# Optimization experiments

Hardware: AMD Instinct MI355X
Metric: run time of the kernel (lower is better)

## Reference

```python
import jax, jax.numpy as jnp
import numpy as np

B, T, D, E, H = 4, 2048, 1024, 4, 8
EPS = 1e-5


def _uniform(k, shape, bound):
    return jax.random.uniform(k, shape, jnp.float32, -bound, bound)


def setup_inputs() -> dict:
    key = jax.random.key(0)
    ks = jax.random.split(key, 12)
    wb = np.sqrt(6.0 / D) / np.sqrt(6.0)  # kaiming_uniform(a=sqrt5) bound ~ 1/sqrt(D)... keep simple
    wb = 1.0 / np.sqrt(D)
    return {
        "x": jax.random.normal(ks[0], (B, T, D), jnp.float32),
        "router_prob": jax.random.uniform(ks[1], (B, T, E), jnp.float32),
        "norm_w": jnp.ones((D,), jnp.float32),
        "norm_b": jnp.zeros((D,), jnp.float32),
        "q_w": _uniform(ks[2], (D, D), wb),
        "q_b": _uniform(ks[3], (D,), wb),
        "k_w": _uniform(ks[4], (D, D), wb),
        "k_b": _uniform(ks[5], (D,), wb),
        "v_w": _uniform(ks[6], (D, D), wb),
        "v_b": _uniform(ks[7], (D,), wb),
        "o_w": _uniform(ks[8], (D, D), wb),
        "o_b": _uniform(ks[9], (D,), wb),
    }


def _layernorm(x, w, b):
    mu = jnp.mean(x, axis=-1, keepdims=True)
    var = jnp.mean(jnp.square(x - mu), axis=-1, keepdims=True)
    return (x - mu) * jax.lax.rsqrt(var + EPS) * w + b


def reference(x, router_prob, norm_w, norm_b, q_w, q_b, k_w, k_b, v_w, v_b, o_w, o_b):
    e_cnt = router_prob.shape[2]
    b, t, d = x.shape
    n = t // e_cnt
    h = H
    scale = d ** (-0.5)  # note: original uses model_dim**-0.5, not head_dim

    qs, ks_, vs = [], [], []
    for e in range(e_cnt):
        xe = x[:, e * n:(e + 1) * n, :]
        xn = _layernorm(xe, norm_w, norm_b)
        m = d // (2 ** e)
        xm = xn[..., :m]  # [b, n, m] matryoshka slice
        # F.linear(xm, W[:, :m], bias): out = xm @ W[:, :m]^T + b -> [b, n, d]
        qs.append(jnp.einsum('bnm,dm->bnd', xm, q_w[:, :m]) + q_b)
        ks_.append(jnp.einsum('bnm,dm->bnd', xm, k_w[:, :m]) + k_b)
        vs.append(jnp.einsum('bnm,dm->bnd', xm, v_w[:, :m]) + v_b)
    q = jnp.concatenate(qs, axis=1)
    k = jnp.concatenate(ks_, axis=1)
    v = jnp.concatenate(vs, axis=1)

    dh = d // h
    q = q.reshape(b, t, h, dh).transpose(0, 2, 1, 3)  # b h t dh
    k = k.reshape(b, t, h, dh).transpose(0, 2, 1, 3)
    v = v.reshape(b, t, h, dh).transpose(0, 2, 1, 3)

    attn = jnp.einsum('bhqd,bhkd->bhqk', q, k) * scale
    attn = jax.nn.softmax(attn, axis=-1)  # dropout = identity in eval
    attn_out = jnp.einsum('bhqk,bhkd->bhqd', attn, v)
    attn_out = attn_out.transpose(0, 2, 1, 3).reshape(b, t, d)

    outs = []
    for e in range(e_cnt):
        sl = slice(e * n, (e + 1) * n)
        m = d // (2 ** e)
        xm = attn_out[:, sl, :m]
        out = jnp.einsum('bnm,om->bno', xm, o_w[:m, :m]) + o_b[:m]  # [b, n, m]
        pad = d - m
        if pad:
            out = jnp.pad(out, ((0, 0), (0, 0), (0, pad)))
        outs.append(out + x[:, sl, :])
    return jnp.concatenate(outs, axis=1)
```

## Files before the change

kernel.cpp:

```cpp
#include <hip/hip_runtime.h>
#include <hip/hip_bf16.h>

#define DEV static __device__ __forceinline__

typedef __attribute__((ext_vector_type(4))) float f32x4;
typedef __attribute__((ext_vector_type(8))) short s16x8;
typedef __attribute__((ext_vector_type(4))) unsigned int u32x4;

constexpr int Bn = 4, Tn = 2048, Dn = 1024, Hn = 8, DH = 128;
constexpr float EPSF = 1e-5f;
constexpr float QSCALE = 0.0450842200277801f;

DEV unsigned short f2bf(float f) {
    unsigned int u = __float_as_uint(f);
    u += 0x7FFF + ((u >> 16) & 1);
    return (unsigned short)(u >> 16);
}

DEV f32x4 mfma16(s16x8 a, s16x8 b, f32x4 c) {
    return __builtin_amdgcn_mfma_f32_16x16x32_bf16(a, b, c, 0, 0, 0);
}

DEV float ex2(float x) {
    float r;
    asm("v_exp_f32 %0, %1" : "=v"(r) : "v"(x));
    return r;
}

DEV unsigned int cvtpk(float lo, float hi) {
    unsigned int r;
    asm("v_cvt_pk_bf16_f32 %0, %1, %2" : "=v"(r) : "v"(lo), "v"(hi));
    return r;
}

typedef __attribute__((address_space(1))) const unsigned int GU32;
typedef __attribute__((address_space(3))) unsigned int LU32;
DEV void gload16(const void* g, void* l) {
    __builtin_amdgcn_global_load_lds((GU32*)g, (LU32*)l, 16, 0, 0);
}

__global__ __launch_bounds__(256) void cvtln_kernel(const float* __restrict__ x,
                                                    const float* __restrict__ w,
                                                    const float* __restrict__ b,
                                                    const float* __restrict__ qw,
                                                    const float* __restrict__ kw,
                                                    const float* __restrict__ vw,
                                                    const float* __restrict__ ow,
                                                    unsigned short* __restrict__ xn,
                                                    unsigned short* __restrict__ wb) {
    int bid = blockIdx.x;
    int tid = threadIdx.x;
    if (bid >= 8192) {
        int base = (bid - 8192) * 1024 + tid * 4;
        #pragma unroll
        for (int j = 0; j < 4; j++) {
            int idx = base + j;
            int sel = idx >> 20;
            int off = idx & (Dn * Dn - 1);
            const float* src = sel == 0 ? qw : sel == 1 ? kw : sel == 2 ? vw : ow;
            wb[idx] = f2bf(src[off]);
        }
        return;
    }
    int tok = bid;
    const float* xp = x + (size_t)tok * Dn;
    float4 v = ((const float4*)xp)[tid];
    float s = v.x + v.y + v.z + v.w;
    float q = v.x * v.x + v.y * v.y + v.z * v.z + v.w * v.w;
    for (int off = 32; off; off >>= 1) {
        s += __shfl_xor(s, off);
        q += __shfl_xor(q, off);
    }
    __shared__ float red[8];
    __shared__ float stats[2];
    int wid = tid >> 6, lane = tid & 63;
    if (lane == 0) { red[wid] = s; red[4 + wid] = q; }
    __syncthreads();
    if (tid == 0) {
        float ts = red[0] + red[1] + red[2] + red[3];
        float tq = red[4] + red[5] + red[6] + red[7];
        float mu = ts / Dn;
        float var = tq / Dn - mu * mu;
        stats[0] = mu;
        stats[1] = rsqrtf(var + EPSF);
    }
    __syncthreads();
    float mu = stats[0], rs = stats[1];
    int c = tid * 4;
    ushort4 o;
    o.x = f2bf((v.x - mu) * rs * w[c + 0] + b[c + 0]);
    o.y = f2bf((v.y - mu) * rs * w[c + 1] + b[c + 1]);
    o.z = f2bf((v.z - mu) * rs * w[c + 2] + b[c + 2]);
    o.w = f2bf((v.w - mu) * rs * w[c + 3] + b[c + 3]);
    ((ushort4*)(xn + (size_t)tok * Dn))[tid] = o;
}

__global__ __launch_bounds__(256) void qkv_gemm(const unsigned short* __restrict__ xn,
                                                const unsigned short* __restrict__ wmat,
                                                const float* __restrict__ qb_,
                                                const float* __restrict__ kb_,
                                                const float* __restrict__ vb_,
                                                unsigned short* __restrict__ outq,
                                                unsigned short* __restrict__ outk,
                                                unsigned short* __restrict__ vt) {
    int rowbase = blockIdx.x * 128;
    int colbase = blockIdx.y * 128;
    int matid = blockIdx.z;
    const unsigned short* W = wmat + (size_t)matid * Dn * Dn;
    const float* bias = matid == 0 ? qb_ : matid == 1 ? kb_ : vb_;
    float oscale = matid == 0 ? QSCALE : 1.0f;
    int e = (rowbase & (Tn - 1)) >> 9;
    int m = Dn >> e;
    int nt = m >> 5;

    __shared__ alignas(16) unsigned short At[3][128 * 32];
    __shared__ alignas(16) unsigned short Bt[3][128 * 32];

    int tid = threadIdx.x;
    int lane = tid & 63, wv = tid >> 6;
    int wr = (wv >> 1) * 64, wc = (wv & 1) * 64;
    int fr = lane & 15, fg = lane >> 4;
    int srow = tid >> 2, scol = (tid & 3) * 8;
    const unsigned short* ga0 = xn + (size_t)(rowbase + srow) * Dn + scol;
    const unsigned short* ga1 = xn + (size_t)(rowbase + 64 + srow) * Dn + scol;
    const unsigned short* gb0 = W + (size_t)(colbase + srow) * Dn + scol;
    const unsigned short* gb1 = W + (size_t)(colbase + 64 + srow) * Dn + scol;

    f32x4 acc[4][4] = {};

    auto STAGE = [&](int tt, int buf) {
        int kk = tt * 32;
        gload16(ga0 + kk, &At[buf][tid * 8]);
        gload16(ga1 + kk, &At[buf][2048 + tid * 8]);
        gload16(gb0 + kk, &Bt[buf][tid * 8]);
        gload16(gb1 + kk, &Bt[buf][2048 + tid * 8]);
    };

    STAGE(0, 0);
    if (nt > 1) STAGE(1, 1);

    int cur = 0, nxt2 = 2;
    for (int t = 0; t < nt; t++) {
        if (t + 1 < nt) { asm volatile("s_waitcnt vmcnt(4)" ::: "memory"); }
        else            { asm volatile("s_waitcnt vmcnt(0)" ::: "memory"); }
        __builtin_amdgcn_s_barrier();
        if (t + 2 < nt) STAGE(t + 2, nxt2);
        s16x8 a[4], b[4];
        #pragma unroll
        for (int i = 0; i < 4; i++) a[i] = *(const s16x8*)&At[cur][(wr + i * 16 + fr) * 32 + fg * 8];
        #pragma unroll
        for (int j = 0; j < 4; j++) b[j] = *(const s16x8*)&Bt[cur][(wc + j * 16 + fr) * 32 + fg * 8];
        #pragma unroll
        for (int i = 0; i < 4; i++)
            #pragma unroll
            for (int j = 0; j < 4; j++) acc[i][j] = mfma16(a[i], b[j], acc[i][j]);
        cur = cur == 2 ? 0 : cur + 1;
        nxt2 = nxt2 == 2 ? 0 : nxt2 + 1;
    }

    if (matid == 2) {
        #pragma unroll
        for (int i = 0; i < 4; i++)
            #pragma unroll
            for (int j = 0; j < 4; j++) {
                int col = colbase + wc + j * 16 + fr;
                float bv = bias[col];
                int row0 = rowbase + wr + i * 16 + fg * 4;
                int bb = row0 >> 11, tl = row0 & (Tn - 1);
                int w32 = tl & 31;
                int tlp = (tl & ~31) | (((w32 >> 2) & 3) * 8 + ((w32 >> 4) & 1) * 4);
                size_t base = (((size_t)bb * Hn + (col >> 7)) * DH + (col & (DH - 1))) * Tn + tlp;
                ushort4 o;
                o.x = f2bf(acc[i][j][0] + bv);
                o.y = f2bf(acc[i][j][1] + bv);
                o.z = f2bf(acc[i][j][2] + bv);
                o.w = f2bf(acc[i][j][3] + bv);
                *(ushort4*)&vt[base] = o;
            }
    } else {
        unsigned short* out = matid == 0 ? outq : outk;
        #pragma unroll
        for (int i = 0; i < 4; i++)
            #pragma unroll
            for (int j = 0; j < 4; j++) {
                int col = colbase + wc + j * 16 + fr;
                float bv = bias[col];
                #pragma unroll
                for (int r = 0; r < 4; r++) {
                    int row = rowbase + wr + i * 16 + fg * 4 + r;
                    out[(size_t)row * Dn + col] = f2bf((acc[i][j][r] + bv) * oscale);
                }
            }
    }
}

__global__ __launch_bounds__(256, 2) void attn_kernel(const unsigned short* __restrict__ Q,
                                                      const unsigned short* __restrict__ K,
                                                      const unsigned short* __restrict__ VT,
                                                      unsigned short* __restrict__ AO) {
    int f = blockIdx.x;
    int qi = f >> 5;
    int bh = f & 31;
    int b = bh >> 3, h = bh & 7;
    int qbase = qi * 128;
    int tid = threadIdx.x;
    int wv = tid >> 6, lane = tid & 63;
    int fr = lane & 15, fg = lane >> 4;

    __shared__ alignas(16) unsigned short Kt[3][32 * 128];
    __shared__ alignas(16) unsigned short Vt[3][64 * 64];

    s16x8 bq[2][4];
    #pragma unroll
    for (int hh = 0; hh < 2; hh++) {
        const size_t qr = ((size_t)b * Tn + qbase + wv * 32 + hh * 16 + fr) * Dn + h * DH;
        #pragma unroll
        for (int c = 0; c < 4; c++) bq[hh][c] = *(const s16x8*)&Q[qr + c * 32 + fg * 8];
    }

    const s16x8 ones = {(short)0x3F80, (short)0x3F80, (short)0x3F80, (short)0x3F80,
                        (short)0x3F80, (short)0x3F80, (short)0x3F80, (short)0x3F80};

    f32x4 acc[2][9] = {};
    float m_run[2] = {-1e30f, -1e30f};

    const unsigned short* Kbase = K + (size_t)b * Tn * Dn + h * DH;
    const unsigned short* Vbase = VT + ((size_t)b * Hn + h) * DH * Tn;

    int k_row_lo = tid >> 4, k_chk = tid & 15;
    int v_row_lo = tid >> 3, v_s = tid & 7;

    auto STAGE = [&](int t) {
        int kb = t * 32;
        int buf = t % 3;
        #pragma unroll
        for (int p = 0; p < 2; p++) {
            int row = p * 16 + k_row_lo;
            int chunk = k_chk ^ (row & 7);
            gload16(Kbase + (size_t)(kb + row) * Dn + chunk * 8,
                    &Kt[buf][p * 2048 + tid * 8]);
        }
        #pragma unroll
        for (int p = 0; p < 2; p++) {
            int row = p * 32 + v_row_lo;
            int c = v_s ^ (row & 7);
            int hi = c >> 2, fgc = c & 3;
            gload16(Vbase + (size_t)(hi * 64 + row) * Tn + kb + fgc * 8,
                    &Vt[buf][p * 2048 + tid * 8]);
        }
    };

    STAGE(0);
    STAGE(1);

    constexpr int NT = Tn / 32;
    int cur = 0;
    for (int t = 0; t < NT; t++) {
        if (t + 1 < NT) { asm volatile("s_waitcnt vmcnt(4)" ::: "memory"); }
        else            { asm volatile("s_waitcnt vmcnt(0)" ::: "memory"); }
        __builtin_amdgcn_s_barrier();
        if (t + 2 < NT) STAGE(t + 2);

        const unsigned short* KtC = &Kt[cur][0];
        const unsigned short* VtC = &Vt[cur][0];

        f32x4 s[2][2] = {};
        __builtin_amdgcn_s_setprio(1);
        #pragma unroll
        for (int c = 0; c < 4; c++) {
            #pragma unroll
            for (int kt = 0; kt < 2; kt++) {
                s16x8 ak = *(const s16x8*)&KtC[(kt * 16 + fr) * 128 +
                                               (((c * 4 + fg) ^ (fr & 7)) * 8)];
                s[0][kt] = mfma16(ak, bq[0][c], s[0][kt]);
                s[1][kt] = mfma16(ak, bq[1][c], s[1][kt]);
            }
        }
        __builtin_amdgcn_s_setprio(0);

        float mx[2];
        #pragma unroll
        for (int hh = 0; hh < 2; hh++) {
            float v = fmaxf(fmaxf(fmaxf(s[hh][0][0], s[hh][0][1]),
                                  fmaxf(s[hh][0][2], s[hh][0][3])),
                            fmaxf(fmaxf(s[hh][1][0], s[hh][1][1]),
                                  fmaxf(s[hh][1][2], s[hh][1][3])));
            v = fmaxf(v, __shfl_xor(v, 16));
            v = fmaxf(v, __shfl_xor(v, 32));
            mx[hh] = v;
        }

        if (!__all(mx[0] - m_run[0] <= 8.0f && mx[1] - m_run[1] <= 8.0f)) {
            #pragma unroll
            for (int hh = 0; hh < 2; hh++) {
                float mnew = fmaxf(m_run[hh], mx[hh]);
                float fsc = ex2(m_run[hh] - mnew);
                float fw[4];
                #pragma unroll
                for (int r = 0; r < 4; r++) fw[r] = __shfl(fsc, fg * 4 + r);
                #pragma unroll
                for (int n = 0; n < 9; n++)
                    #pragma unroll
                    for (int r = 0; r < 4; r++) acc[hh][n][r] *= fw[r];
                m_run[hh] = mnew;
            }
        }

        s16x8 pa[2];
        #pragma unroll
        for (int hh = 0; hh < 2; hh++) {
            float p[8];
            #pragma unroll
            for (int kt = 0; kt < 2; kt++)
                #pragma unroll
                for (int r = 0; r < 4; r++) p[kt * 4 + r] = ex2(s[hh][kt][r] - m_run[hh]);
            u32x4 pw;
            pw.x = cvtpk(p[0], p[1]);
            pw.y = cvtpk(p[2], p[3]);
            pw.z = cvtpk(p[4], p[5]);
            pw.w = cvtpk(p[6], p[7]);
            pa[hh] = __builtin_bit_cast(s16x8, pw);
        }

        __builtin_amdgcn_s_setprio(1);
        #pragma unroll
        for (int n = 0; n < 8; n++) {
            int row = (n & 3) * 16 + fr;
            int hi = n >> 2;
            s16x8 bv = *(const s16x8*)&VtC[row * 64 +
                                           (((hi * 4 + fg) ^ (row & 7)) * 8)];
            acc[0][n] = mfma16(pa[0], bv, acc[0][n]);
            acc[1][n] = mfma16(pa[1], bv, acc[1][n]);
        }
        acc[0][8] = mfma16(pa[0], ones, acc[0][8]);
        acc[1][8] = mfma16(pa[1], ones, acc[1][8]);
        __builtin_amdgcn_s_setprio(0);

        cur = cur == 2 ? 0 : cur + 1;
    }

    #pragma unroll
    for (int hh = 0; hh < 2; hh++) {
        float rl[4];
        #pragma unroll
        for (int r = 0; r < 4; r++) rl[r] = 1.0f / acc[hh][8][r];
        size_t orow0 = ((size_t)b * Tn + qbase + wv * 32 + hh * 16) * Dn + h * DH;
        for (int n = 0; n < 8; n++)
            for (int r = 0; r < 4; r++) {
                float v = acc[hh][n][r] * rl[r];
                AO[orow0 + (size_t)(fg * 4 + r) * Dn + n * 16 + fr] = f2bf(v);
            }
    }
}

__global__ __launch_bounds__(256) void oproj_gemm(const unsigned short* __restrict__ A,
                                                  const unsigned short* __restrict__ W,
                                                  const float* __restrict__ bias,
                                                  const float* __restrict__ x,
                                                  float* __restrict__ out) {
    int rowbase = blockIdx.x * 128;
    int colbase = blockIdx.y * 128;
    int e = (rowbase & (Tn - 1)) >> 9;
    int m = Dn >> e;
    int tid = threadIdx.x;

    if (colbase >= m) {
        #pragma unroll
        for (int i = 0; i < 16; i++) {
            int idx = i * 256 + tid;
            int r = idx >> 5, c4 = (idx & 31) * 4;
            size_t g = (size_t)(rowbase + r) * Dn + colbase + c4;
            *(float4*)&out[g] = *(const float4*)&x[g];
        }
        return;
    }

    __shared__ alignas(16) unsigned short At[3][128 * 32];
    __shared__ alignas(16) unsigned short Bt[3][128 * 32];
    int lane = tid & 63, wv = tid >> 6;
    int wr = (wv >> 1) * 64, wc = (wv & 1) * 64;
    int fr = lane & 15, fg = lane >> 4;
    int srow = tid >> 2, scol = (tid & 3) * 8;
    const unsigned short* ga0 = A + (size_t)(rowbase + srow) * Dn + scol;
    const unsigned short* ga1 = A + (size_t)(rowbase + 64 + srow) * Dn + scol;
    const unsigned short* gb0 = W + (size_t)(colbase + srow) * Dn + scol;
    const unsigned short* gb1 = W + (size_t)(colbase + 64 + srow) * Dn + scol;
    int nt = m >> 5;

    f32x4 acc[4][4] = {};

    auto STAGE = [&](int tt, int buf) {
        int kk = tt * 32;
        gload16(ga0 + kk, &At[buf][tid * 8]);
        gload16(ga1 + kk, &At[buf][2048 + tid * 8]);
        gload16(gb0 + kk, &Bt[buf][tid * 8]);
        gload16(gb1 + kk, &Bt[buf][2048 + tid * 8]);
    };

    STAGE(0, 0);
    if (nt > 1) STAGE(1, 1);

    int cur = 0, nxt2 = 2;
    for (int t = 0; t < nt; t++) {
        if (t + 1 < nt) { asm volatile("s_waitcnt vmcnt(4)" ::: "memory"); }
        else            { asm volatile("s_waitcnt vmcnt(0)" ::: "memory"); }
        __builtin_amdgcn_s_barrier();
        if (t + 2 < nt) STAGE(t + 2, nxt2);
        s16x8 a[4], b[4];
        #pragma unroll
        for (int i = 0; i < 4; i++) a[i] = *(const s16x8*)&At[cur][(wr + i * 16 + fr) * 32 + fg * 8];
        #pragma unroll
        for (int j = 0; j < 4; j++) b[j] = *(const s16x8*)&Bt[cur][(wc + j * 16 + fr) * 32 + fg * 8];
        #pragma unroll
        for (int i = 0; i < 4; i++)
            #pragma unroll
            for (int j = 0; j < 4; j++) acc[i][j] = mfma16(a[i], b[j], acc[i][j]);
        cur = cur == 2 ? 0 : cur + 1;
        nxt2 = nxt2 == 2 ? 0 : nxt2 + 1;
    }

    #pragma unroll
    for (int i = 0; i < 4; i++)
        #pragma unroll
        for (int j = 0; j < 4; j++) {
            int col = colbase + wc + j * 16 + fr;
            float bv = bias[col];
            #pragma unroll
            for (int r = 0; r < 4; r++) {
                int row = rowbase + wr + i * 16 + fg * 4 + r;
                size_t g = (size_t)row * Dn + col;
                out[g] = acc[i][j][r] + bv + x[g];
            }
        }
}

extern "C" void kernel_launch(void* const* d_in, const int* in_sizes, int n_in,
                              void* d_out, int out_size, void* d_ws, size_t ws_size,
                              hipStream_t stream) {
    const float* x   = (const float*)d_in[0];
    const float* nw  = (const float*)d_in[2];
    const float* nb  = (const float*)d_in[3];
    const float* qw  = (const float*)d_in[4];
    const float* qb_ = (const float*)d_in[5];
    const float* kw  = (const float*)d_in[6];
    const float* kb_ = (const float*)d_in[7];
    const float* vw  = (const float*)d_in[8];
    const float* vb_ = (const float*)d_in[9];
    const float* ow  = (const float*)d_in[10];
    const float* ob_ = (const float*)d_in[11];
    float* out = (float*)d_out;

    unsigned short* ws = (unsigned short*)d_ws;
    const size_t NTOK = (size_t)Bn * Tn;
    unsigned short* xn = ws;
    unsigned short* qd = xn + NTOK * Dn;
    unsigned short* kd = qd + NTOK * Dn;
    unsigned short* vt = kd + NTOK * Dn;
    unsigned short* ao = vt + NTOK * Dn;
    unsigned short* wb = ao + NTOK * Dn;

    hipLaunchKernelGGL(cvtln_kernel, dim3(12288), dim3(256), 0, stream,
                       x, nw, nb, qw, kw, vw, ow, xn, wb);
    hipLaunchKernelGGL(qkv_gemm, dim3(64, 8, 3), dim3(256), 0, stream,
                       xn, wb, qb_, kb_, vb_, qd, kd, vt);
    hipLaunchKernelGGL(attn_kernel, dim3(512), dim3(256), 0, stream, qd, kd, vt, ao);
    hipLaunchKernelGGL(oproj_gemm, dim3(64, 8), dim3(256), 0, stream,
                       ao, wb + (size_t)3 * Dn * Dn, ob_, x, out);
}
```

Baseline: 200.3 us.

## Enlarge attention tiles to 256 queries and 128-key double-buffered KV stages

The attention kernel now runs 512-thread blocks that each own 256 query rows, so there are half as many blocks and each K/V tile loaded into LDS is reused by twice as many queries. The key step grows from 32 to 128 keys and the triple buffer with fine-grained vmcnt waits becomes a double buffer with a full __syncthreads per step. V is laid out as a plain 128x128 swizzled tile. The aim is to cut global K/V traffic and per-step barrier and softmax bookkeeping. In exchange it uses about 128KB of LDS, allows only one block per CU, and gives coarser load/compute overlap.

```diff
diff --git a/kernel.cpp b/kernel.cpp
--- a/kernel.cpp
+++ b/kernel.cpp
@@ -194,7 +194,7 @@
     }
 }
 
-__global__ __launch_bounds__(256, 2) void attn_kernel(const unsigned short* __restrict__ Q,
+__global__ __launch_bounds__(512, 1) void attn_kernel(const unsigned short* __restrict__ Q,
                                                       const unsigned short* __restrict__ K,
                                                       const unsigned short* __restrict__ VT,
                                                       unsigned short* __restrict__ AO) {
@@ -202,13 +202,13 @@
     int qi = f >> 5;
     int bh = f & 31;
     int b = bh >> 3, h = bh & 7;
-    int qbase = qi * 128;
+    int qbase = qi * 256;
     int tid = threadIdx.x;
     int wv = tid >> 6, lane = tid & 63;
     int fr = lane & 15, fg = lane >> 4;
 
-    __shared__ alignas(16) unsigned short Kt[3][32 * 128];
-    __shared__ alignas(16) unsigned short Vt[3][64 * 64];
+    __shared__ alignas(16) unsigned short Kt[2][128 * 128];
+    __shared__ alignas(16) unsigned short Vt[2][128 * 128];
 
     s16x8 bq[2][4];
     #pragma unroll
@@ -227,49 +227,43 @@
     const unsigned short* Kbase = K + (size_t)b * Tn * Dn + h * DH;
     const unsigned short* Vbase = VT + ((size_t)b * Hn + h) * DH * Tn;
 
-    int k_row_lo = tid >> 4, k_chk = tid & 15;
-    int v_row_lo = tid >> 3, v_s = tid & 7;
-
-    auto STAGE = [&](int t) {
-        int kb = t * 32;
-        int buf = t % 3;
-        #pragma unroll
-        for (int p = 0; p < 2; p++) {
-            int row = p * 16 + k_row_lo;
-            int chunk = k_chk ^ (row & 7);
+    int s_row_lo = tid >> 4, s_chk = tid & 15;
+
+    auto STAGE = [&](int t, int buf) {
+        int kb = t * 128;
+        #pragma unroll
+        for (int p = 0; p < 4; p++) {
+            int row = p * 32 + s_row_lo;
+            int chunk = s_chk ^ (row & 7);
             gload16(Kbase + (size_t)(kb + row) * Dn + chunk * 8,
-                    &Kt[buf][p * 2048 + tid * 8]);
-        }
-        #pragma unroll
-        for (int p = 0; p < 2; p++) {
-            int row = p * 32 + v_row_lo;
-            int c = v_s ^ (row & 7);
-            int hi = c >> 2, fgc = c & 3;
-            gload16(Vbase + (size_t)(hi * 64 + row) * Tn + kb + fgc * 8,
-                    &Vt[buf][p * 2048 + tid * 8]);
+                    &Kt[buf][p * 4096 + tid * 8]);
+        }
+        #pragma unroll
+        for (int p = 0; p < 4; p++) {
+            int row = p * 32 + s_row_lo;
+            int chunk = s_chk ^ (row & 15);
+            gload16(Vbase + (size_t)row * Tn + kb + chunk * 8,
+                    &Vt[buf][p * 4096 + tid * 8]);
         }
     };
 
-    STAGE(0);
-    STAGE(1);
-
-    constexpr int NT = Tn / 32;
-    int cur = 0;
+    STAGE(0, 0);
+    __syncthreads();
+
+    constexpr int NT = Tn / 128;
     for (int t = 0; t < NT; t++) {
-        if (t + 1 < NT) { asm volatile("s_waitcnt vmcnt(4)" ::: "memory"); }
-        else            { asm volatile("s_waitcnt vmcnt(0)" ::: "memory"); }
-        __builtin_amdgcn_s_barrier();
-        if (t + 2 < NT) STAGE(t + 2);
+        int cur = t & 1;
+        if (t < NT - 1) STAGE(t + 1, cur ^ 1);
 
         const unsigned short* KtC = &Kt[cur][0];
         const unsigned short* VtC = &Vt[cur][0];
 
-        f32x4 s[2][2] = {};
+        f32x4 s[2][8] = {};
         __builtin_amdgcn_s_setprio(1);
         #pragma unroll
         for (int c = 0; c < 4; c++) {
             #pragma unroll
-            for (int kt = 0; kt < 2; kt++) {
+            for (int kt = 0; kt < 8; kt++) {
                 s16x8 ak = *(const s16x8*)&KtC[(kt * 16 + fr) * 128 +
                                                (((c * 4 + fg) ^ (fr & 7)) * 8)];
                 s[0][kt] = mfma16(ak, bq[0][c], s[0][kt]);
@@ -281,10 +275,11 @@
         float mx[2];
         #pragma unroll
         for (int hh = 0; hh < 2; hh++) {
-            float v = fmaxf(fmaxf(fmaxf(s[hh][0][0], s[hh][0][1]),
-                                  fmaxf(s[hh][0][2], s[hh][0][3])),
-                            fmaxf(fmaxf(s[hh][1][0], s[hh][1][1]),
-                                  fmaxf(s[hh][1][2], s[hh][1][3])));
+            float v = s[hh][0][0];
+            #pragma unroll
+            for (int kt = 0; kt < 8; kt++)
+                #pragma unroll
+                for (int r = 0; r < 4; r++) v = fmaxf(v, s[hh][kt][r]);
             v = fmaxf(v, __shfl_xor(v, 16));
             v = fmaxf(v, __shfl_xor(v, 32));
             mx[hh] = v;
@@ -306,37 +301,44 @@
             }
         }
 
-        s16x8 pa[2];
+        s16x8 pa[2][4];
         #pragma unroll
         for (int hh = 0; hh < 2; hh++) {
-            float p[8];
-            #pragma unroll
-            for (int kt = 0; kt < 2; kt++)
-                #pragma unroll
-                for (int r = 0; r < 4; r++) p[kt * 4 + r] = ex2(s[hh][kt][r] - m_run[hh]);
-            u32x4 pw;
-            pw.x = cvtpk(p[0], p[1]);
-            pw.y = cvtpk(p[2], p[3]);
-            pw.z = cvtpk(p[4], p[5]);
-            pw.w = cvtpk(p[6], p[7]);
-            pa[hh] = __builtin_bit_cast(s16x8, pw);
+            #pragma unroll
+            for (int ks = 0; ks < 4; ks++) {
+                float p0 = ex2(s[hh][ks * 2 + 0][0] - m_run[hh]);
+                float p1 = ex2(s[hh][ks * 2 + 0][1] - m_run[hh]);
+                float p2 = ex2(s[hh][ks * 2 + 0][2] - m_run[hh]);
+                float p3 = ex2(s[hh][ks * 2 + 0][3] - m_run[hh]);
+                float p4 = ex2(s[hh][ks * 2 + 1][0] - m_run[hh]);
+                float p5 = ex2(s[hh][ks * 2 + 1][1] - m_run[hh]);
+                float p6 = ex2(s[hh][ks * 2 + 1][2] - m_run[hh]);
+                float p7 = ex2(s[hh][ks * 2 + 1][3] - m_run[hh]);
+                u32x4 pw;
+                pw.x = cvtpk(p0, p1);
+                pw.y = cvtpk(p2, p3);
+                pw.z = cvtpk(p4, p5);
+                pw.w = cvtpk(p6, p7);
+                pa[hh][ks] = __builtin_bit_cast(s16x8, pw);
+            }
         }
 
         __builtin_amdgcn_s_setprio(1);
         #pragma unroll
-        for (int n = 0; n < 8; n++) {
-            int row = (n & 3) * 16 + fr;
-            int hi = n >> 2;
-            s16x8 bv = *(const s16x8*)&VtC[row * 64 +
-                                           (((hi * 4 + fg) ^ (row & 7)) * 8)];
-            acc[0][n] = mfma16(pa[0], bv, acc[0][n]);
-            acc[1][n] = mfma16(pa[1], bv, acc[1][n]);
-        }
-        acc[0][8] = mfma16(pa[0], ones, acc[0][8]);
-        acc[1][8] = mfma16(pa[1], ones, acc[1][8]);
+        for (int ks = 0; ks < 4; ks++) {
+            #pragma unroll
+            for (int n = 0; n < 8; n++) {
+                int row = n * 16 + fr;
+                s16x8 bv = *(const s16x8*)&VtC[row * 128 +
+                                               (((ks * 4 + fg) ^ (row & 15)) * 8)];
+                acc[0][n] = mfma16(pa[0][ks], bv, acc[0][n]);
+                acc[1][n] = mfma16(pa[1][ks], bv, acc[1][n]);
+            }
+            acc[0][8] = mfma16(pa[0][ks], ones, acc[0][8]);
+            acc[1][8] = mfma16(pa[1][ks], ones, acc[1][8]);
+        }
         __builtin_amdgcn_s_setprio(0);
-
-        cur = cur == 2 ? 0 : cur + 1;
+        __syncthreads();
     }
 
     #pragma unroll
@@ -463,7 +465,7 @@
                        x, nw, nb, qw, kw, vw, ow, xn, wb);
     hipLaunchKernelGGL(qkv_gemm, dim3(64, 8, 3), dim3(256), 0, stream,
                        xn, wb, qb_, kb_, vb_, qd, kd, vt);
-    hipLaunchKernelGGL(attn_kernel, dim3(512), dim3(256), 0, stream, qd, kd, vt, ao);
+    hipLaunchKernelGGL(attn_kernel, dim3(256), dim3(512), 0, stream, qd, kd, vt, ao);
     hipLaunchKernelGGL(oproj_gemm, dim3(64, 8), dim3(256), 0, stream,
                        ao, wb + (size_t)3 * Dn * Dn, ob_, x, out);
 }
```

Measured after the change: 185.3 us, median of 2. 1.08x faster.

## Split key range across two wave groups in attention and merge partial softmax

Applied to the files above, without the earlier changes.

Attention blocks now use 512 threads. Two 4-wave halves each process half of the key sequence for the same 128 queries with double-buffered LDS staging, then combine their partial outputs and normalisers via shared memory using max-rescaling. This is meant to raise the number of waves working per CU and halve the serial loop length per wave. In exchange it replaces the 3-stage vmcnt-based prefetch pipeline with a barrier-synchronised double buffer and adds a reduction epilogue, which may reduce load/compute overlap.

```diff
diff --git a/kernel.cpp b/kernel.cpp
--- a/kernel.cpp
+++ b/kernel.cpp
@@ -194,7 +194,7 @@
     }
 }
 
-__global__ __launch_bounds__(256, 2) void attn_kernel(const unsigned short* __restrict__ Q,
+__global__ __launch_bounds__(512, 4) void attn_kernel(const unsigned short* __restrict__ Q,
                                                       const unsigned short* __restrict__ K,
                                                       const unsigned short* __restrict__ VT,
                                                       unsigned short* __restrict__ AO) {
@@ -204,16 +204,18 @@
     int b = bh >> 3, h = bh & 7;
     int qbase = qi * 128;
     int tid = threadIdx.x;
-    int wv = tid >> 6, lane = tid & 63;
+    int wv = tid >> 6;
+    int g = wv & 3;
+    int half = wv >> 2;
+    int lane = tid & 63;
     int fr = lane & 15, fg = lane >> 4;
 
-    __shared__ alignas(16) unsigned short Kt[3][32 * 128];
-    __shared__ alignas(16) unsigned short Vt[3][64 * 64];
+    __shared__ alignas(16) unsigned char smem[65536];
 
     s16x8 bq[2][4];
     #pragma unroll
     for (int hh = 0; hh < 2; hh++) {
-        const size_t qr = ((size_t)b * Tn + qbase + wv * 32 + hh * 16 + fr) * Dn + h * DH;
+        const size_t qr = ((size_t)b * Tn + qbase + g * 32 + hh * 16 + fr) * Dn + h * DH;
         #pragma unroll
         for (int c = 0; c < 4; c++) bq[hh][c] = *(const s16x8*)&Q[qr + c * 32 + fg * 8];
     }
@@ -227,18 +229,25 @@
     const unsigned short* Kbase = K + (size_t)b * Tn * Dn + h * DH;
     const unsigned short* Vbase = VT + ((size_t)b * Hn + h) * DH * Tn;
 
-    int k_row_lo = tid >> 4, k_chk = tid & 15;
-    int v_row_lo = tid >> 3, v_s = tid & 7;
-
-    auto STAGE = [&](int t) {
-        int kb = t * 32;
-        int buf = t % 3;
+    int tl = tid & 255;
+    int k_row_lo = tl >> 4, k_chk = tl & 15;
+    int v_row_lo = tl >> 3, v_s = tl & 7;
+
+    unsigned short* kbuf0 = (unsigned short*)(smem + (half * 2 + 0) * 8192);
+    unsigned short* kbuf1 = (unsigned short*)(smem + (half * 2 + 1) * 8192);
+    unsigned short* vbuf0 = (unsigned short*)(smem + 32768 + (half * 2 + 0) * 8192);
+    unsigned short* vbuf1 = (unsigned short*)(smem + 32768 + (half * 2 + 1) * 8192);
+
+    auto STAGE = [&](int t, int buf) {
+        int kb = half * 1024 + t * 32;
+        unsigned short* kdst = buf ? kbuf1 : kbuf0;
+        unsigned short* vdst = buf ? vbuf1 : vbuf0;
         #pragma unroll
         for (int p = 0; p < 2; p++) {
             int row = p * 16 + k_row_lo;
             int chunk = k_chk ^ (row & 7);
             gload16(Kbase + (size_t)(kb + row) * Dn + chunk * 8,
-                    &Kt[buf][p * 2048 + tid * 8]);
+                    kdst + p * 2048 + tl * 8);
         }
         #pragma unroll
         for (int p = 0; p < 2; p++) {
@@ -246,23 +255,20 @@
             int c = v_s ^ (row & 7);
             int hi = c >> 2, fgc = c & 3;
             gload16(Vbase + (size_t)(hi * 64 + row) * Tn + kb + fgc * 8,
-                    &Vt[buf][p * 2048 + tid * 8]);
+                    vdst + p * 2048 + tl * 8);
         }
     };
 
-    STAGE(0);
-    STAGE(1);
-
-    constexpr int NT = Tn / 32;
-    int cur = 0;
+    STAGE(0, 0);
+    __syncthreads();
+
+    constexpr int NT = 1024 / 32;
     for (int t = 0; t < NT; t++) {
-        if (t + 1 < NT) { asm volatile("s_waitcnt vmcnt(4)" ::: "memory"); }
-        else            { asm volatile("s_waitcnt vmcnt(0)" ::: "memory"); }
-        __builtin_amdgcn_s_barrier();
-        if (t + 2 < NT) STAGE(t + 2);
-
-        const unsigned short* KtC = &Kt[cur][0];
-        const unsigned short* VtC = &Vt[cur][0];
+        int cur = t & 1;
+        if (t < NT - 1) STAGE(t + 1, cur ^ 1);
+
+        const unsigned short* KtC = cur ? kbuf1 : kbuf0;
+        const unsigned short* VtC = cur ? vbuf1 : vbuf0;
 
         f32x4 s[2][2] = {};
         __builtin_amdgcn_s_setprio(1);
@@ -335,21 +341,47 @@
         acc[0][8] = mfma16(pa[0], ones, acc[0][8]);
         acc[1][8] = mfma16(pa[1], ones, acc[1][8]);
         __builtin_amdgcn_s_setprio(0);
-
-        cur = cur == 2 ? 0 : cur + 1;
-    }
-
+        __syncthreads();
+    }
+
+    float* mbuf = (float*)smem;
     #pragma unroll
-    for (int hh = 0; hh < 2; hh++) {
-        float rl[4];
-        #pragma unroll
-        for (int r = 0; r < 4; r++) rl[r] = 1.0f / acc[hh][8][r];
-        size_t orow0 = ((size_t)b * Tn + qbase + wv * 32 + hh * 16) * Dn + h * DH;
-        for (int n = 0; n < 8; n++)
+    for (int p = 0; p < 2; p++) {
+        __syncthreads();
+        if (half == 0) {
+            float* dst = mbuf + (g * 64 + lane) * 40;
+            #pragma unroll
+            for (int n = 0; n < 9; n++) *(f32x4*)(dst + n * 4) = acc[p][n];
+            #pragma unroll
+            for (int r = 0; r < 4; r++) dst[36 + r] = __shfl(m_run[p], fg * 4 + r);
+        }
+        __syncthreads();
+        if (half == 1) {
+            const float* src = mbuf + (g * 64 + lane) * 40;
+            float mB[4];
+            #pragma unroll
+            for (int r = 0; r < 4; r++) mB[r] = __shfl(m_run[p], fg * 4 + r);
+            float fA[4], fB[4], rl[4];
+            #pragma unroll
             for (int r = 0; r < 4; r++) {
-                float v = acc[hh][n][r] * rl[r];
-                AO[orow0 + (size_t)(fg * 4 + r) * Dn + n * 16 + fr] = f2bf(v);
-            }
+                float mA = src[36 + r];
+                float M = fmaxf(mA, mB[r]);
+                fA[r] = ex2(mA - M);
+                fB[r] = ex2(mB[r] - M);
+                float l = fA[r] * src[32 + r] + fB[r] * acc[p][8][r];
+                rl[r] = 1.0f / l;
+            }
+            size_t orow0 = ((size_t)b * Tn + qbase + g * 32 + p * 16) * Dn + h * DH;
+            #pragma unroll
+            for (int n = 0; n < 8; n++) {
+                f32x4 oA = *(const f32x4*)(src + n * 4);
+                #pragma unroll
+                for (int r = 0; r < 4; r++) {
+                    float v = (fA[r] * oA[r] + fB[r] * acc[p][n][r]) * rl[r];
+                    AO[orow0 + (size_t)(fg * 4 + r) * Dn + n * 16 + fr] = f2bf(v);
+                }
+            }
+        }
     }
 }
 
@@ -463,7 +495,7 @@
                        x, nw, nb, qw, kw, vw, ow, xn, wb);
     hipLaunchKernelGGL(qkv_gemm, dim3(64, 8, 3), dim3(256), 0, stream,
                        xn, wb, qb_, kb_, vb_, qd, kd, vt);
-    hipLaunchKernelGGL(attn_kernel, dim3(512), dim3(256), 0, stream, qd, kd, vt, ao);
+    hipLaunchKernelGGL(attn_kernel, dim3(512), dim3(512), 0, stream, qd, kd, vt, ao);
     hipLaunchKernelGGL(oproj_gemm, dim3(64, 8), dim3(256), 0, stream,
                        ao, wb + (size_t)3 * Dn * Dn, ob_, x, out);
 }
```

Measured after the change: 269.3 us. +34.5%, slower.
